# Kernel tuning notes

Measured on AMD Instinct MI355X. Metric: run time of the kernel, lower is better.

Reference implementation:

```python
import jax, jax.numpy as jnp
import numpy as np

B, C, Himg, Wimg = 4, 256, 64, 64
HID = 256
K = 8
EPS_NORM = 1e-12
BN_EPS = 1e-5


def setup_inputs() -> dict:
    key = jax.random.key(0)
    ks = jax.random.split(key, 14)
    s = lambda fan: 1.0 / np.sqrt(fan)
    inp = {
        "features": jax.random.normal(ks[0], (B, C, Himg, Wimg), dtype=jnp.float32),
        # HypergraphConv 0: theta (C->HID), phi (HID->HID). Weights stored [in,out].
        "theta0_w": jax.random.normal(ks[1], (C, HID), dtype=jnp.float32) * s(C),
        "theta0_b": jnp.zeros((HID,), jnp.float32),
        "phi0_w": jax.random.normal(ks[2], (HID, HID), dtype=jnp.float32) * s(HID),
        "phi0_b": jnp.zeros((HID,), jnp.float32),
        # HypergraphConv 1: theta (HID->HID), phi (HID->HID)
        "theta1_w": jax.random.normal(ks[3], (HID, HID), dtype=jnp.float32) * s(HID),
        "theta1_b": jnp.zeros((HID,), jnp.float32),
        "phi1_w": jax.random.normal(ks[4], (HID, HID), dtype=jnp.float32) * s(HID),
        "phi1_b": jnp.zeros((HID,), jnp.float32),
        # out_proj: 1x1 conv HID->C, stored as [HID, C]
        "proj_w": jax.random.normal(ks[5], (HID, C), dtype=jnp.float32) * s(HID),
        "proj_b": jnp.zeros((C,), jnp.float32),
        # BatchNorm2d affine params
        "bn_gamma": jnp.ones((C,), jnp.float32),
        "bn_beta": jnp.zeros((C,), jnp.float32),
    }
    return inp


def _build_hypergraph(features):
    # features: [B, C, H, W] -> nodes [B, N, C]; incidence from batch 0 only
    b, c, h, w = features.shape
    n = h * w
    feat_flat = features.reshape(b, c, n).transpose(0, 2, 1)  # [B, N, C]
    f0 = feat_flat[0]  # [N, C] (original computes full-batch similarity but uses [0])
    f0n = f0 / jnp.maximum(jnp.linalg.norm(f0, axis=-1, keepdims=True), EPS_NORM)
    sim = f0n @ f0n.T  # [N, N]
    _, idx = jax.lax.top_k(sim, K)  # [N, K]
    rows = idx.reshape(-1)
    cols = jnp.repeat(jnp.arange(n), K)
    Hm = jnp.zeros((n, n), jnp.float32).at[rows, cols].set(1.0)  # [N, E=N]
    # L1 column normalization (F.normalize p=1 dim=0)
    Hn = Hm / jnp.maximum(Hm.sum(axis=0, keepdims=True), EPS_NORM)
    return Hn, feat_flat


def _hconv(x, Hn, tw, tb, pw, pb):
    # x: [B, N, Cin]
    xt = x @ tw + tb  # [B, N, Cout]
    ef = jnp.einsum('ne,bnc->bec', Hn, xt)  # H^T @ x_theta -> edge feats
    xp = ef @ pw + pb  # [B, E, Cout]
    return jnp.einsum('ne,bec->bnc', Hn, xp)  # H @ x_phi


def reference(features, theta0_w, theta0_b, phi0_w, phi0_b,
              theta1_w, theta1_b, phi1_w, phi1_b,
              proj_w, proj_b, bn_gamma, bn_beta):
    b, c, h, w = features.shape
    Hn, x = _build_hypergraph(features)
    x = jax.nn.relu(_hconv(x, Hn, theta0_w, theta0_b, phi0_w, phi0_b))
    x = jax.nn.relu(_hconv(x, Hn, theta1_w, theta1_b, phi1_w, phi1_b)) + x
    # back to [B, HID, H, W] then 1x1 conv
    x = x.transpose(0, 2, 1).reshape(b, HID, h, w)
    x = jnp.einsum('bihw,io->bohw', x, proj_w) + proj_b[None, :, None, None]
    # BatchNorm2d (training mode: batch statistics, biased variance)
    mean = x.mean(axis=(0, 2, 3))
    var = x.var(axis=(0, 2, 3))
    xn = (x - mean[None, :, None, None]) * jax.lax.rsqrt(var + BN_EPS)[None, :, None, None]
    xn = xn * bn_gamma[None, :, None, None] + bn_beta[None, :, None, None]
    return features + xn
```

## Files before the change

### kernel.cpp

```cpp
#include <hip/hip_runtime.h>

namespace {

constexpr int NB = 4;
constexpr int NC = 256;
constexpr int NN = 4096;

typedef __attribute__((ext_vector_type(8))) short bf8;
typedef __attribute__((ext_vector_type(4))) float f4;
typedef unsigned short ushort_t;
typedef unsigned long long ull;

__device__ __forceinline__ float bf2f(unsigned short u) {
  return __uint_as_float(((unsigned)u) << 16);
}
__device__ __forceinline__ unsigned short f2bf(float f) {
  unsigned x = __float_as_uint(f);
  return (unsigned short)((x + 0x7FFFu + ((x >> 16) & 1u)) >> 16);
}

__device__ __forceinline__ unsigned enc_f(float f) {
  unsigned u = __float_as_uint(f);
  return (u & 0x80000000u) ? ~u : (u | 0x80000000u);
}

__device__ __forceinline__ void ins8(ull* b, ull k) {
  if (k <= b[7]) return;
  b[7] = k;
#pragma unroll
  for (int p = 7; p >= 1; --p) {
    if (b[p] > b[p-1]) { ull t = b[p]; b[p] = b[p-1]; b[p-1] = t; }
  }
}

__global__ __launch_bounds__(256) void norm_kernel(const float* __restrict__ feat,
                                                   float* __restrict__ inv,
                                                   int* __restrict__ counts,
                                                   float* __restrict__ bnsum) {
  int n = blockIdx.x * 256 + threadIdx.x;
  counts[n] = 0;
  if (n < 2 * NC) bnsum[n] = 0.f;
  float ss = 0.f;
  for (int c = 0; c < NC; ++c) { float v = feat[(size_t)c * NN + n]; ss = fmaf(v, v, ss); }
  inv[n] = 1.f / fmaxf(sqrtf(ss), 1e-12f);
}

__global__ __launch_bounds__(256) void xpose_split_kernel(const float* __restrict__ feat,
                                                          const float* __restrict__ inv,
                                                          unsigned short* __restrict__ Xhi,
                                                          unsigned short* __restrict__ Xlo) {
  __shared__ float tile[64][65];
  int n0 = blockIdx.x * 64, c0 = blockIdx.y * 64;
  int tid = threadIdx.x;
#pragma unroll
  for (int i = 0; i < 4; ++i) {
    int u = tid + i * 256; int cr = u >> 4, q = u & 15;
    float4 v = *(const float4*)&feat[(size_t)(c0 + cr) * NN + n0 + q * 4];
    tile[cr][q*4+0] = v.x; tile[cr][q*4+1] = v.y; tile[cr][q*4+2] = v.z; tile[cr][q*4+3] = v.w;
  }
  __syncthreads();
#pragma unroll
  for (int i = 0; i < 4; ++i) {
    int u = tid + i * 256; int nr = u >> 4, q = u & 15;
    float iv = inv[n0 + nr];
    ushort4 h, l;
    float x0 = tile[q*4+0][nr] * iv, x1 = tile[q*4+1][nr] * iv;
    float x2 = tile[q*4+2][nr] * iv, x3 = tile[q*4+3][nr] * iv;
    h.x = f2bf(x0); l.x = f2bf(x0 - bf2f(h.x));
    h.y = f2bf(x1); l.y = f2bf(x1 - bf2f(h.y));
    h.z = f2bf(x2); l.z = f2bf(x2 - bf2f(h.z));
    h.w = f2bf(x3); l.w = f2bf(x3 - bf2f(h.w));
    size_t o = (size_t)(n0 + nr) * NC + c0 + q * 4;
    *(ushort4*)&Xhi[o] = h;
    *(ushort4*)&Xlo[o] = l;
  }
}

__global__ __launch_bounds__(256) void wcvt_kernel(const float* __restrict__ w0,
                                                   const float* __restrict__ w1,
                                                   const float* __restrict__ w2,
                                                   const float* __restrict__ w3,
                                                   const float* __restrict__ w4,
                                                   unsigned short* __restrict__ Wt) {
  __shared__ float tile[64][65];
  int z = blockIdx.z;
  const float* W = (z == 0) ? w0 : (z == 1) ? w1 : (z == 2) ? w2 : (z == 3) ? w3 : w4;
  int k0 = blockIdx.x * 64, n0 = blockIdx.y * 64;
  int tid = threadIdx.x;
#pragma unroll
  for (int i = 0; i < 4; ++i) {
    int u = tid + i * 256; int kr = u >> 4, q = u & 15;
    float4 v = *(const float4*)&W[(size_t)(k0 + kr) * NC + n0 + q * 4];
    tile[kr][q*4+0] = v.x; tile[kr][q*4+1] = v.y; tile[kr][q*4+2] = v.z; tile[kr][q*4+3] = v.w;
  }
  __syncthreads();
#pragma unroll
  for (int i = 0; i < 4; ++i) {
    int u = tid + i * 256; int nr = u >> 4, q = u & 15;
    ushort4 o;
    o.x = f2bf(tile[q*4+0][nr]); o.y = f2bf(tile[q*4+1][nr]);
    o.z = f2bf(tile[q*4+2][nr]); o.w = f2bf(tile[q*4+3][nr]);
    *(ushort4*)&Wt[(size_t)z * 65536 + (size_t)(n0 + nr) * NC + k0 + q * 4] = o;
  }
}

__global__ __launch_bounds__(256) void feat2bf_kernel(const float* __restrict__ feat,
                                                      unsigned short* __restrict__ xin) {
  __shared__ float tile[64][65];
  int n0 = blockIdx.x * 64, c0 = blockIdx.y * 64, b = blockIdx.z;
  int tid = threadIdx.x;
#pragma unroll
  for (int i = 0; i < 4; ++i) {
    int u = tid + i * 256; int cr = u >> 4, q = u & 15;
    float4 v = *(const float4*)&feat[((size_t)b * NC + c0 + cr) * NN + n0 + q * 4];
    tile[cr][q*4+0] = v.x; tile[cr][q*4+1] = v.y; tile[cr][q*4+2] = v.z; tile[cr][q*4+3] = v.w;
  }
  __syncthreads();
#pragma unroll
  for (int i = 0; i < 4; ++i) {
    int u = tid + i * 256; int nr = u >> 4, q = u & 15;
    ushort4 o;
    o.x = f2bf(tile[q*4+0][nr]); o.y = f2bf(tile[q*4+1][nr]);
    o.z = f2bf(tile[q*4+2][nr]); o.w = f2bf(tile[q*4+3][nr]);
    *(ushort4*)&xin[((size_t)(b << 12) + n0 + nr) * NC + c0 + q * 4] = o;
  }
}

__global__ __launch_bounds__(256) void simtop_kernel(const unsigned short* __restrict__ Xhi,
                                                     const unsigned short* __restrict__ Xlo,
                                                     ull* __restrict__ cand) {
  __shared__ __align__(16) char lds[73728];
  ushort_t (*sAh)[72] = (ushort_t(*)[72])(lds);
  ushort_t (*sAl)[72] = (ushort_t(*)[72])(lds + 18432);
  ushort_t (*sBh)[72] = (ushort_t(*)[72])(lds + 36864);
  ushort_t (*sBl)[72] = (ushort_t(*)[72])(lds + 55296);
  float    (*simT)[132] = (float(*)[132])(lds);
  ull* scratch = (ull*)(lds);

  int tid = threadIdx.x, wave = tid >> 6, lane = tid & 63;
  int wm = wave >> 1, wn = wave & 1;
  int m0 = blockIdx.y * 128, n0 = blockIdx.x * 128;
  f4 acc[4][4];
#pragma unroll
  for (int i = 0; i < 4; ++i)
#pragma unroll
    for (int j = 0; j < 4; ++j) acc[i][j] = (f4){0.f, 0.f, 0.f, 0.f};

  for (int k0 = 0; k0 < NC; k0 += 64) {
#pragma unroll
    for (int i = 0; i < 4; ++i) {
      int u = tid + i * 256; int r = u >> 3, q = u & 7;
      size_t am = (size_t)(m0 + r) * NC + k0 + q * 8;
      size_t an = (size_t)(n0 + r) * NC + k0 + q * 8;
      *(uint4*)&sAh[r][q*8] = *(const uint4*)&Xhi[am];
      *(uint4*)&sAl[r][q*8] = *(const uint4*)&Xlo[am];
      *(uint4*)&sBh[r][q*8] = *(const uint4*)&Xhi[an];
      *(uint4*)&sBl[r][q*8] = *(const uint4*)&Xlo[an];
    }
    __syncthreads();
#pragma unroll
    for (int ks = 0; ks < 2; ++ks) {
      bf8 ah[4], al[4];
#pragma unroll
      for (int mf = 0; mf < 4; ++mf) {
        ah[mf] = *(const bf8*)&sAh[wm*64 + mf*16 + (lane & 15)][ks*32 + (lane >> 4)*8];
        al[mf] = *(const bf8*)&sAl[wm*64 + mf*16 + (lane & 15)][ks*32 + (lane >> 4)*8];
      }
#pragma unroll
      for (int nf = 0; nf < 4; ++nf) {
        bf8 bh = *(const bf8*)&sBh[wn*64 + nf*16 + (lane & 15)][ks*32 + (lane >> 4)*8];
        bf8 bl = *(const bf8*)&sBl[wn*64 + nf*16 + (lane & 15)][ks*32 + (lane >> 4)*8];
#pragma unroll
        for (int mf = 0; mf < 4; ++mf) {
          acc[mf][nf] = __builtin_amdgcn_mfma_f32_16x16x32_bf16(ah[mf], bh, acc[mf][nf], 0, 0, 0);
          acc[mf][nf] = __builtin_amdgcn_mfma_f32_16x16x32_bf16(ah[mf], bl, acc[mf][nf], 0, 0, 0);
          acc[mf][nf] = __builtin_amdgcn_mfma_f32_16x16x32_bf16(al[mf], bh, acc[mf][nf], 0, 0, 0);
        }
      }
    }
    __syncthreads();
  }

#pragma unroll
  for (int mf = 0; mf < 4; ++mf) {
#pragma unroll
    for (int nf = 0; nf < 4; ++nf) {
      int cl = wn*64 + nf*16 + (lane & 15);
#pragma unroll
      for (int r = 0; r < 4; ++r) {
        simT[wm*64 + mf*16 + (lane >> 4)*4 + r][cl] = acc[mf][nf][r];
      }
    }
  }
  __syncthreads();

  int r_loc = tid >> 1, h = tid & 1;
  const float* rowp = &simT[r_loc][h * 64];
  ull b8[8] = {0,0,0,0,0,0,0,0};
#pragma unroll
  for (int i = 0; i < 16; ++i) {
    float4 v = *(const float4*)(rowp + i * 4);
    int jb = n0 + h*64 + i*4;
    ins8(b8, ((ull)enc_f(v.x) << 32) | (ull)(0xFFFFFFFFu - (unsigned)(jb + 0)));
    ins8(b8, ((ull)enc_f(v.y) << 32) | (ull)(0xFFFFFFFFu - (unsigned)(jb + 1)));
    ins8(b8, ((ull)enc_f(v.z) << 32) | (ull)(0xFFFFFFFFu - (unsigned)(jb + 2)));
    ins8(b8, ((ull)enc_f(v.w) << 32) | (ull)(0xFFFFFFFFu - (unsigned)(jb + 3)));
  }
  __syncthreads();
  if (h) {
#pragma unroll
    for (int k = 0; k < 8; ++k) scratch[r_loc * 8 + k] = b8[k];
  }
  __syncthreads();
  if (!h) {
#pragma unroll
    for (int k = 0; k < 8; ++k) ins8(b8, scratch[r_loc * 8 + k]);
    ull* dst = cand + (size_t)(m0 + r_loc) * 256 + blockIdx.x * 8;
#pragma unroll
    for (int k = 0; k < 8; ++k) dst[k] = b8[k];
  }
}

__global__ __launch_bounds__(256) void merge_kernel(const ull* __restrict__ cand,
                                                    int* __restrict__ idx8,
                                                    int* __restrict__ counts) {
  int row = blockIdx.x * 256 + threadIdx.x;
  const ull* cp = cand + (size_t)row * 256;
  ull b8[8] = {0,0,0,0,0,0,0,0};
  for (int g = 0; g < 32; ++g) {
#pragma unroll 1
    for (int k = 0; k < 8; ++k) {
      ull key = cp[g * 8 + k];
      if (key <= b8[7]) break;
      ins8(b8, key);
    }
  }
#pragma unroll
  for (int k = 0; k < 8; ++k) {
    int j = (int)(0xFFFFFFFFu - (unsigned)(b8[k] & 0xFFFFFFFFull));
    idx8[row * 8 + k] = j;
    atomicAdd(&counts[j], 1);
  }
}

__global__ __launch_bounds__(256) void scan_kernel(const int* __restrict__ counts,
                                                   int* __restrict__ offsets,
                                                   int* __restrict__ cursor) {
  __shared__ int ssum[256];
  __shared__ int sbase[257];
  int t = threadIdx.x;
  int loc[16];
  int s = 0;
#pragma unroll
  for (int i = 0; i < 16; ++i) { loc[i] = s; s += counts[t*16 + i]; }
  ssum[t] = s;
  __syncthreads();
  if (t == 0) {
    int acc = 0;
    for (int i = 0; i < 256; ++i) { sbase[i] = acc; acc += ssum[i]; }
    sbase[256] = acc;
  }
  __syncthreads();
  int b0 = sbase[t];
#pragma unroll
  for (int i = 0; i < 16; ++i) {
    int off = b0 + loc[i];
    offsets[t*16 + i] = off;
    cursor [t*16 + i] = off;
  }
  if (t == 0) offsets[NN] = sbase[256];
}

__global__ __launch_bounds__(256) void fill_kernel(const int* __restrict__ idx8,
                                                   int* __restrict__ cursor,
                                                   int* __restrict__ edgelist) {
  int t = blockIdx.x * 256 + threadIdx.x;
  int n = idx8[t];
  int pos = atomicAdd(&cursor[n], 1);
  edgelist[pos] = t >> 3;
}

template<int OUTF32, int BNS>
__global__ __launch_bounds__(512) void gemm_bf16_kernel(const unsigned short* __restrict__ A,
                                                        const unsigned short* __restrict__ Wt,
                                                        const float* __restrict__ bias,
                                                        void* __restrict__ outp,
                                                        float* __restrict__ bnsum) {
  __shared__ ushort_t sA[128][72];
  __shared__ ushort_t sB[128][72];
  int tid = threadIdx.x, wave = tid >> 6, lane = tid & 63;
  int wm = wave >> 2, wn = wave & 3;
  int n0 = blockIdx.x * 128, m0 = blockIdx.y * 128;
  f4 acc[4][2];
#pragma unroll
  for (int i = 0; i < 4; ++i)
#pragma unroll
    for (int j = 0; j < 2; ++j) acc[i][j] = (f4){0.f, 0.f, 0.f, 0.f};

  for (int k0 = 0; k0 < NC; k0 += 64) {
#pragma unroll
    for (int i = 0; i < 2; ++i) {
      int u = tid + i * 512; int r = u >> 3, q = u & 7;
      *(uint4*)&sA[r][q*8] = *(const uint4*)&A [(size_t)(m0 + r) * NC + k0 + q * 8];
      *(uint4*)&sB[r][q*8] = *(const uint4*)&Wt[(size_t)(n0 + r) * NC + k0 + q * 8];
    }
    __syncthreads();
#pragma unroll
    for (int ks = 0; ks < 2; ++ks) {
      bf8 a[4], b[2];
#pragma unroll
      for (int mf = 0; mf < 4; ++mf)
        a[mf] = *(const bf8*)&sA[wm*64 + mf*16 + (lane & 15)][ks*32 + (lane >> 4)*8];
#pragma unroll
      for (int nf = 0; nf < 2; ++nf)
        b[nf] = *(const bf8*)&sB[wn*32 + nf*16 + (lane & 15)][ks*32 + (lane >> 4)*8];
#pragma unroll
      for (int nf = 0; nf < 2; ++nf)
#pragma unroll
        for (int mf = 0; mf < 4; ++mf)
          acc[mf][nf] = __builtin_amdgcn_mfma_f32_16x16x32_bf16(a[mf], b[nf], acc[mf][nf], 0, 0, 0);
    }
    __syncthreads();
  }
#pragma unroll
  for (int nf = 0; nf < 2; ++nf) {
    int n = n0 + wn*32 + nf*16 + (lane & 15);
    float bi = bias[n];
    float s1 = 0.f, s2 = 0.f;
#pragma unroll
    for (int mf = 0; mf < 4; ++mf) {
#pragma unroll
      for (int r = 0; r < 4; ++r) {
        int m = m0 + wm*64 + mf*16 + (lane >> 4)*4 + r;
        float v = acc[mf][nf][r] + bi;
        if (OUTF32) ((float*)outp)[(size_t)m * NC + n] = v;
        else ((unsigned short*)outp)[(size_t)m * NC + n] = f2bf(v);
        if (BNS) { s1 += v; s2 = fmaf(v, v, s2); }
      }
    }
    if (BNS) {
      s1 += __shfl_xor(s1, 16); s1 += __shfl_xor(s1, 32);
      s2 += __shfl_xor(s2, 16); s2 += __shfl_xor(s2, 32);
      if (lane < 16) {
        atomicAdd(&bnsum[n], s1);
        atomicAdd(&bnsum[NC + n], s2);
      }
    }
  }
}

__global__ __launch_bounds__(256) void gather_kernel(const unsigned short* __restrict__ xt,
                                                     const int* __restrict__ idx8,
                                                     unsigned short* __restrict__ ef) {
  int b = blockIdx.y;
  int e = blockIdx.x * 4 + (threadIdx.x >> 6);
  int lane = threadIdx.x & 63;
  float s0 = 0, s1 = 0, s2 = 0, s3 = 0;
  const int* ip = &idx8[e * 8];
#pragma unroll
  for (int k = 0; k < 8; ++k) {
    int n = ip[k];
    uint2 v = *(const uint2*)&xt[((size_t)((b << 12) + n)) * NC + lane * 4];
    s0 += bf2f((unsigned short)(v.x & 0xFFFF)); s1 += bf2f((unsigned short)(v.x >> 16));
    s2 += bf2f((unsigned short)(v.y & 0xFFFF)); s3 += bf2f((unsigned short)(v.y >> 16));
  }
  uint2 o;
  o.x = (unsigned)f2bf(s0 * 0.125f) | ((unsigned)f2bf(s1 * 0.125f) << 16);
  o.y = (unsigned)f2bf(s2 * 0.125f) | ((unsigned)f2bf(s3 * 0.125f) << 16);
  *(uint2*)&ef[((size_t)((b << 12) + e)) * NC + lane * 4] = o;
}

template<int MODE>
__global__ __launch_bounds__(256) void scatter_kernel(const unsigned short* __restrict__ xp,
                                                      const int* __restrict__ offsets,
                                                      const int* __restrict__ edgelist,
                                                      const unsigned short* __restrict__ res,
                                                      unsigned short* __restrict__ outb) {
  int b = blockIdx.y;
  int n = blockIdx.x * 4 + (threadIdx.x >> 6);
  int lane = threadIdx.x & 63;
  int s0i = offsets[n], s1i = offsets[n + 1];
  float s0 = 0, s1 = 0, s2 = 0, s3 = 0;
  for (int j = s0i; j < s1i; ++j) {
    int e = edgelist[j];
    uint2 v = *(const uint2*)&xp[((size_t)((b << 12) + e)) * NC + lane * 4];
    s0 += bf2f((unsigned short)(v.x & 0xFFFF)); s1 += bf2f((unsigned short)(v.x >> 16));
    s2 += bf2f((unsigned short)(v.y & 0xFFFF)); s3 += bf2f((unsigned short)(v.y >> 16));
  }
  s0 = fmaxf(s0 * 0.125f, 0.f); s1 = fmaxf(s1 * 0.125f, 0.f);
  s2 = fmaxf(s2 * 0.125f, 0.f); s3 = fmaxf(s3 * 0.125f, 0.f);
  size_t o = ((size_t)((b << 12) + n)) * NC + lane * 4;
  if (MODE == 1) {
    uint2 v = *(const uint2*)&res[o];
    s0 += bf2f((unsigned short)(v.x & 0xFFFF)); s1 += bf2f((unsigned short)(v.x >> 16));
    s2 += bf2f((unsigned short)(v.y & 0xFFFF)); s3 += bf2f((unsigned short)(v.y >> 16));
  }
  uint2 ov;
  ov.x = (unsigned)f2bf(s0) | ((unsigned)f2bf(s1) << 16);
  ov.y = (unsigned)f2bf(s2) | ((unsigned)f2bf(s3) << 16);
  *(uint2*)&outb[o] = ov;
}

__global__ __launch_bounds__(256) void final_kernel(const float* __restrict__ y,
                                                    const float* __restrict__ feat,
                                                    const float* __restrict__ bnsum,
                                                    const float* __restrict__ gam,
                                                    const float* __restrict__ bet,
                                                    float* __restrict__ out) {
  __shared__ float tile[64][65];
  __shared__ float sa_[64], sb_[64];
  int n0 = blockIdx.x * 64;
  int c0 = blockIdx.y * 64;
  int b  = blockIdx.z;
  int tid = threadIdx.x;
  if (tid < 64) {
    const float invn = 1.f / (float)(NB * NN);
    int c = c0 + tid;
    float mean = bnsum[c] * invn;
    float var  = bnsum[NC + c] * invn - mean * mean;
    float a = gam[c] * rsqrtf(var + 1e-5f);
    sa_[tid] = a;
    sb_[tid] = bet[c] - mean * a;
  }
  int n_l = tid >> 2;
  int q   = tid & 3;
  const float4* y4 = (const float4*)y;
#pragma unroll
  for (int i = 0; i < 4; ++i) {
    int cl = q * 16 + i * 4;
    float4 v = y4[(size_t)(b * NN + n0 + n_l) * 64 + ((c0 + cl) >> 2)];
    tile[n_l][cl+0] = v.x; tile[n_l][cl+1] = v.y; tile[n_l][cl+2] = v.z; tile[n_l][cl+3] = v.w;
  }
  __syncthreads();
  int cl2 = tid >> 6;
  int nl2 = tid & 63;
#pragma unroll
  for (int p = 0; p < 16; ++p) {
    int ci = p * 4 + cl2;
    float a = sa_[ci], bb = sb_[ci];
    size_t o = (size_t)b * (NC * NN) + (size_t)(c0 + ci) * NN + n0 + nl2;
    out[o] = feat[o] + fmaf(a, tile[nl2][ci], bb);
  }
}

}

extern "C" void kernel_launch(void* const* d_in, const int* in_sizes, int n_in,
                              void* d_out, int out_size, void* d_ws, size_t ws_size,
                              hipStream_t stream) {
  (void)in_sizes; (void)n_in; (void)out_size; (void)ws_size;
  const float* feat = (const float*)d_in[0];
  const float* t0w  = (const float*)d_in[1];
  const float* t0b  = (const float*)d_in[2];
  const float* p0w  = (const float*)d_in[3];
  const float* p0b  = (const float*)d_in[4];
  const float* t1w  = (const float*)d_in[5];
  const float* t1b  = (const float*)d_in[6];
  const float* p1w  = (const float*)d_in[7];
  const float* p1b  = (const float*)d_in[8];
  const float* pw   = (const float*)d_in[9];
  const float* pb   = (const float*)d_in[10];
  const float* gam  = (const float*)d_in[11];
  const float* bet  = (const float*)d_in[12];
  float* out = (float*)d_out;

  char* ws = (char*)d_ws;
  float*          y   = (float*)ws;
  unsigned short* xin = (unsigned short*)(ws + (16u << 20));
  unsigned short* xt  = (unsigned short*)(ws + (24u << 20));
  unsigned short* ef  = (unsigned short*)(ws + (32u << 20));
  unsigned short* xp  = (unsigned short*)(ws + (40u << 20));
  unsigned short* x1  = (unsigned short*)(ws + (48u << 20));
  unsigned short* x2  = (unsigned short*)(ws + (56u << 20));
  unsigned short* Xhi = (unsigned short*)(ws + (64u << 20));
  unsigned short* Xlo = (unsigned short*)(ws + (66u << 20));
  ull*            cand = (ull*)(ws + (68u << 20));
  char* sm = ws + (76u << 20);
  unsigned short* Wt  = (unsigned short*)sm;
  int*   idx8     = (int*)(sm + 655360);
  int*   counts   = (int*)(sm + 786432);
  int*   offsets  = (int*)(sm + 802816);
  int*   cursor   = (int*)(sm + 819456);
  int*   edgelist = (int*)(sm + 835840);
  float* inv      = (float*)(sm + 966912);
  float* bnsum    = (float*)(sm + 983296);

  norm_kernel<<<NN / 256, 256, 0, stream>>>(feat, inv, counts, bnsum);
  xpose_split_kernel<<<dim3(64, 4), 256, 0, stream>>>(feat, inv, Xhi, Xlo);
  wcvt_kernel<<<dim3(4, 4, 5), 256, 0, stream>>>(t0w, p0w, t1w, p1w, pw, Wt);
  feat2bf_kernel<<<dim3(64, 4, 4), 256, 0, stream>>>(feat, xin);

  simtop_kernel<<<dim3(32, 32), 256, 0, stream>>>(Xhi, Xlo, cand);
  merge_kernel<<<16, 256, 0, stream>>>(cand, idx8, counts);
  scan_kernel<<<1, 256, 0, stream>>>(counts, offsets, cursor);
  fill_kernel<<<128, 256, 0, stream>>>(idx8, cursor, edgelist);

  gemm_bf16_kernel<0,0><<<dim3(2, 128), 512, 0, stream>>>(xin, Wt + 0*65536, t0b, xt, nullptr);
  gather_kernel<<<dim3(1024, 4), 256, 0, stream>>>(xt, idx8, ef);
  gemm_bf16_kernel<0,0><<<dim3(2, 128), 512, 0, stream>>>(ef, Wt + 1*65536, p0b, xp, nullptr);
  scatter_kernel<0><<<dim3(1024, 4), 256, 0, stream>>>(xp, offsets, edgelist, nullptr, x1);
  gemm_bf16_kernel<0,0><<<dim3(2, 128), 512, 0, stream>>>(x1, Wt + 2*65536, t1b, xt, nullptr);
  gather_kernel<<<dim3(1024, 4), 256, 0, stream>>>(xt, idx8, ef);
  gemm_bf16_kernel<0,0><<<dim3(2, 128), 512, 0, stream>>>(ef, Wt + 3*65536, p1b, xp, nullptr);
  scatter_kernel<1><<<dim3(1024, 4), 256, 0, stream>>>(xp, offsets, edgelist, x1, x2);
  gemm_bf16_kernel<1,1><<<dim3(2, 128), 512, 0, stream>>>(x2, Wt + 4*65536, pb, y, bnsum);

  final_kernel<<<dim3(64, 4, 4), 256, 0, stream>>>(y, feat, bnsum, gam, bet, out);
}
```

Before: 369.5 us.

## Exploit similarity symmetry, fuse gather into GEMM, swizzle LDS, parallelize top-k merge

The similarity/top-k kernel now computes only the upper-triangular tiles and uses each tile twice, once for row candidates and once for column candidates via a transposed scan, which halves the split-bf16 MFMA work. It moves to 512-thread blocks with XOR-swizzled LDS and a shuffle-based 4-way top-8 merge. The merge kernel splits each row across 8 lanes and combines them with shuffles. The edge-feature gather is fused into the A-tile load of the phi GEMM, which removes two kernels and the ef round trip. Risks include extra per-block gather latency inside the GEMM, because each tile is re-gathered for every N block, and serial column scans on LDS.

```diff
diff --git a/kernel.cpp b/kernel.cpp
--- a/kernel.cpp
+++ b/kernel.cpp
@@ -18,7 +18,6 @@
   unsigned x = __float_as_uint(f);
   return (unsigned short)((x + 0x7FFFu + ((x >> 16) & 1u)) >> 16);
 }
-
 __device__ __forceinline__ unsigned enc_f(float f) {
   unsigned u = __float_as_uint(f);
   return (u & 0x80000000u) ? ~u : (u | 0x80000000u);
@@ -30,6 +29,25 @@
 #pragma unroll
   for (int p = 7; p >= 1; --p) {
     if (b[p] > b[p-1]) { ull t = b[p]; b[p] = b[p-1]; b[p-1] = t; }
+  }
+}
+
+__device__ __forceinline__ ull shfl_xor_ull(ull v, int mask) {
+  unsigned lo = (unsigned)(v & 0xFFFFFFFFull), hi = (unsigned)(v >> 32);
+  lo = (unsigned)__shfl_xor((int)lo, mask);
+  hi = (unsigned)__shfl_xor((int)hi, mask);
+  return ((ull)hi << 32) | (ull)lo;
+}
+
+template<int MAXS>
+__device__ __forceinline__ void shfl_merge8(ull* b) {
+#pragma unroll
+  for (int s = 1; s <= MAXS; s <<= 1) {
+    ull tmp[8];
+#pragma unroll
+    for (int k = 0; k < 8; ++k) tmp[k] = shfl_xor_ull(b[k], s);
+#pragma unroll
+    for (int k = 0; k < 8; ++k) ins8(b, tmp[k]);
   }
 }
 
@@ -126,7 +144,7 @@
   }
 }
 
-__global__ __launch_bounds__(256) void simtop_kernel(const unsigned short* __restrict__ Xhi,
+__global__ __launch_bounds__(512) void simtop_kernel(const unsigned short* __restrict__ Xhi,
                                                      const unsigned short* __restrict__ Xlo,
                                                      ull* __restrict__ cand) {
   __shared__ __align__(16) char lds[73728];
@@ -135,99 +153,123 @@
   ushort_t (*sBh)[72] = (ushort_t(*)[72])(lds + 36864);
   ushort_t (*sBl)[72] = (ushort_t(*)[72])(lds + 55296);
   float    (*simT)[132] = (float(*)[132])(lds);
-  ull* scratch = (ull*)(lds);
 
   int tid = threadIdx.x, wave = tid >> 6, lane = tid & 63;
-  int wm = wave >> 1, wn = wave & 1;
-  int m0 = blockIdx.y * 128, n0 = blockIdx.x * 128;
-  f4 acc[4][4];
+  int wm = wave >> 2, wn = wave & 3;
+  int bid = blockIdx.x;
+  int pi = (int)((sqrtf(8.f * (float)bid + 1.f) - 1.f) * 0.5f);
+  while ((pi + 1) * (pi + 2) / 2 <= bid) ++pi;
+  while (pi * (pi + 1) / 2 > bid) --pi;
+  int pj = bid - pi * (pi + 1) / 2;
+  int m0 = pj * 128, n0 = pi * 128;
+
+  f4 acc[4][2];
 #pragma unroll
   for (int i = 0; i < 4; ++i)
 #pragma unroll
-    for (int j = 0; j < 4; ++j) acc[i][j] = (f4){0.f, 0.f, 0.f, 0.f};
+    for (int j = 0; j < 2; ++j) acc[i][j] = (f4){0.f, 0.f, 0.f, 0.f};
 
   for (int k0 = 0; k0 < NC; k0 += 64) {
 #pragma unroll
-    for (int i = 0; i < 4; ++i) {
-      int u = tid + i * 256; int r = u >> 3, q = u & 7;
+    for (int i = 0; i < 2; ++i) {
+      int u = tid + i * 512; int r = u >> 3, q = u & 7;
+      int qp = (q ^ ((r >> 1) & 7)) * 8;
       size_t am = (size_t)(m0 + r) * NC + k0 + q * 8;
       size_t an = (size_t)(n0 + r) * NC + k0 + q * 8;
-      *(uint4*)&sAh[r][q*8] = *(const uint4*)&Xhi[am];
-      *(uint4*)&sAl[r][q*8] = *(const uint4*)&Xlo[am];
-      *(uint4*)&sBh[r][q*8] = *(const uint4*)&Xhi[an];
-      *(uint4*)&sBl[r][q*8] = *(const uint4*)&Xlo[an];
+      *(uint4*)&sAh[r][qp] = *(const uint4*)&Xhi[am];
+      *(uint4*)&sAl[r][qp] = *(const uint4*)&Xlo[am];
+      *(uint4*)&sBh[r][qp] = *(const uint4*)&Xhi[an];
+      *(uint4*)&sBl[r][qp] = *(const uint4*)&Xlo[an];
     }
     __syncthreads();
 #pragma unroll
     for (int ks = 0; ks < 2; ++ks) {
-      bf8 ah[4], al[4];
+      int qr = ks * 4 + (lane >> 4);
+      bf8 ah[4], al[4], bh[2], bl[2];
 #pragma unroll
       for (int mf = 0; mf < 4; ++mf) {
-        ah[mf] = *(const bf8*)&sAh[wm*64 + mf*16 + (lane & 15)][ks*32 + (lane >> 4)*8];
-        al[mf] = *(const bf8*)&sAl[wm*64 + mf*16 + (lane & 15)][ks*32 + (lane >> 4)*8];
-      }
-#pragma unroll
-      for (int nf = 0; nf < 4; ++nf) {
-        bf8 bh = *(const bf8*)&sBh[wn*64 + nf*16 + (lane & 15)][ks*32 + (lane >> 4)*8];
-        bf8 bl = *(const bf8*)&sBl[wn*64 + nf*16 + (lane & 15)][ks*32 + (lane >> 4)*8];
+        int rr = wm*64 + mf*16 + (lane & 15);
+        int qp = (qr ^ ((rr >> 1) & 7)) * 8;
+        ah[mf] = *(const bf8*)&sAh[rr][qp];
+        al[mf] = *(const bf8*)&sAl[rr][qp];
+      }
+#pragma unroll
+      for (int nf = 0; nf < 2; ++nf) {
+        int rr = wn*32 + nf*16 + (lane & 15);
+        int qp = (qr ^ ((rr >> 1) & 7)) * 8;
+        bh[nf] = *(const bf8*)&sBh[rr][qp];
+        bl[nf] = *(const bf8*)&sBl[rr][qp];
+      }
+#pragma unroll
+      for (int nf = 0; nf < 2; ++nf)
 #pragma unroll
         for (int mf = 0; mf < 4; ++mf) {
-          acc[mf][nf] = __builtin_amdgcn_mfma_f32_16x16x32_bf16(ah[mf], bh, acc[mf][nf], 0, 0, 0);
-          acc[mf][nf] = __builtin_amdgcn_mfma_f32_16x16x32_bf16(ah[mf], bl, acc[mf][nf], 0, 0, 0);
-          acc[mf][nf] = __builtin_amdgcn_mfma_f32_16x16x32_bf16(al[mf], bh, acc[mf][nf], 0, 0, 0);
+          acc[mf][nf] = __builtin_amdgcn_mfma_f32_16x16x32_bf16(ah[mf], bh[nf], acc[mf][nf], 0, 0, 0);
+          acc[mf][nf] = __builtin_amdgcn_mfma_f32_16x16x32_bf16(ah[mf], bl[nf], acc[mf][nf], 0, 0, 0);
+          acc[mf][nf] = __builtin_amdgcn_mfma_f32_16x16x32_bf16(al[mf], bh[nf], acc[mf][nf], 0, 0, 0);
         }
-      }
     }
     __syncthreads();
   }
 
 #pragma unroll
-  for (int mf = 0; mf < 4; ++mf) {
-#pragma unroll
-    for (int nf = 0; nf < 4; ++nf) {
-      int cl = wn*64 + nf*16 + (lane & 15);
-#pragma unroll
-      for (int r = 0; r < 4; ++r) {
+  for (int mf = 0; mf < 4; ++mf)
+#pragma unroll
+    for (int nf = 0; nf < 2; ++nf) {
+      int cl = wn*32 + nf*16 + (lane & 15);
+#pragma unroll
+      for (int r = 0; r < 4; ++r)
         simT[wm*64 + mf*16 + (lane >> 4)*4 + r][cl] = acc[mf][nf][r];
-      }
-    }
-  }
-  __syncthreads();
-
-  int r_loc = tid >> 1, h = tid & 1;
-  const float* rowp = &simT[r_loc][h * 64];
-  ull b8[8] = {0,0,0,0,0,0,0,0};
-#pragma unroll
-  for (int i = 0; i < 16; ++i) {
-    float4 v = *(const float4*)(rowp + i * 4);
-    int jb = n0 + h*64 + i*4;
-    ins8(b8, ((ull)enc_f(v.x) << 32) | (ull)(0xFFFFFFFFu - (unsigned)(jb + 0)));
-    ins8(b8, ((ull)enc_f(v.y) << 32) | (ull)(0xFFFFFFFFu - (unsigned)(jb + 1)));
-    ins8(b8, ((ull)enc_f(v.z) << 32) | (ull)(0xFFFFFFFFu - (unsigned)(jb + 2)));
-    ins8(b8, ((ull)enc_f(v.w) << 32) | (ull)(0xFFFFFFFFu - (unsigned)(jb + 3)));
-  }
-  __syncthreads();
-  if (h) {
-#pragma unroll
-    for (int k = 0; k < 8; ++k) scratch[r_loc * 8 + k] = b8[k];
-  }
-  __syncthreads();
-  if (!h) {
-#pragma unroll
-    for (int k = 0; k < 8; ++k) ins8(b8, scratch[r_loc * 8 + k]);
-    ull* dst = cand + (size_t)(m0 + r_loc) * 256 + blockIdx.x * 8;
-#pragma unroll
-    for (int k = 0; k < 8; ++k) dst[k] = b8[k];
+    }
+  __syncthreads();
+
+  {
+    int rrow = tid >> 2, q4 = tid & 3;
+    ull b8[8] = {0,0,0,0,0,0,0,0};
+#pragma unroll
+    for (int i = 0; i < 8; ++i) {
+      int cofs = q4 * 32 + (((i + q4 * 2) & 7)) * 4;
+      float4 v = *(const float4*)&simT[rrow][cofs];
+      int jb = n0 + cofs;
+      ins8(b8, ((ull)enc_f(v.x) << 32) | (ull)(0xFFFFFFFFu - (unsigned)(jb + 0)));
+      ins8(b8, ((ull)enc_f(v.y) << 32) | (ull)(0xFFFFFFFFu - (unsigned)(jb + 1)));
+      ins8(b8, ((ull)enc_f(v.z) << 32) | (ull)(0xFFFFFFFFu - (unsigned)(jb + 2)));
+      ins8(b8, ((ull)enc_f(v.w) << 32) | (ull)(0xFFFFFFFFu - (unsigned)(jb + 3)));
+    }
+    shfl_merge8<2>(b8);
+    if (q4 == 0) {
+      ull* dst = cand + (size_t)(m0 + rrow) * 256 + pi * 8;
+#pragma unroll
+      for (int k = 0; k < 8; ++k) dst[k] = b8[k];
+    }
+  }
+
+  if (pi != pj) {
+    int ccol = tid >> 2, seg = tid & 3;
+    ull c8[8] = {0,0,0,0,0,0,0,0};
+    for (int i = 0; i < 32; ++i) {
+      int rr = seg * 32 + ((i + seg) & 31);
+      float v = simT[rr][ccol];
+      int jb = m0 + rr;
+      ins8(c8, ((ull)enc_f(v) << 32) | (ull)(0xFFFFFFFFu - (unsigned)jb));
+    }
+    shfl_merge8<2>(c8);
+    if (seg == 0) {
+      ull* dst = cand + (size_t)(n0 + ccol) * 256 + pj * 8;
+#pragma unroll
+      for (int k = 0; k < 8; ++k) dst[k] = c8[k];
+    }
   }
 }
 
 __global__ __launch_bounds__(256) void merge_kernel(const ull* __restrict__ cand,
                                                     int* __restrict__ idx8,
                                                     int* __restrict__ counts) {
-  int row = blockIdx.x * 256 + threadIdx.x;
-  const ull* cp = cand + (size_t)row * 256;
+  int t = blockIdx.x * 256 + threadIdx.x;
+  int row = t >> 3, part = t & 7;
+  const ull* cp = cand + (size_t)row * 256 + part * 32;
   ull b8[8] = {0,0,0,0,0,0,0,0};
-  for (int g = 0; g < 32; ++g) {
+  for (int g = 0; g < 4; ++g) {
 #pragma unroll 1
     for (int k = 0; k < 8; ++k) {
       ull key = cp[g * 8 + k];
@@ -235,11 +277,14 @@
       ins8(b8, key);
     }
   }
-#pragma unroll
-  for (int k = 0; k < 8; ++k) {
-    int j = (int)(0xFFFFFFFFu - (unsigned)(b8[k] & 0xFFFFFFFFull));
-    idx8[row * 8 + k] = j;
-    atomicAdd(&counts[j], 1);
+  shfl_merge8<4>(b8);
+  if (part == 0) {
+#pragma unroll
+    for (int k = 0; k < 8; ++k) {
+      int j = (int)(0xFFFFFFFFu - (unsigned)(b8[k] & 0xFFFFFFFFull));
+      idx8[row * 8 + k] = j;
+      atomicAdd(&counts[j], 1);
+    }
   }
 }
 
@@ -280,17 +325,27 @@
   edgelist[pos] = t >> 3;
 }
 
-template<int OUTF32, int BNS>
+template<int OUTF32, int BNS, int GATHER>
 __global__ __launch_bounds__(512) void gemm_bf16_kernel(const unsigned short* __restrict__ A,
                                                         const unsigned short* __restrict__ Wt,
                                                         const float* __restrict__ bias,
                                                         void* __restrict__ outp,
-                                                        float* __restrict__ bnsum) {
+                                                        float* __restrict__ bnsum,
+                                                        const int* __restrict__ idx8) {
   __shared__ ushort_t sA[128][72];
   __shared__ ushort_t sB[128][72];
+  __shared__ int sIdx[128][8];
   int tid = threadIdx.x, wave = tid >> 6, lane = tid & 63;
   int wm = wave >> 2, wn = wave & 3;
   int n0 = blockIdx.x * 128, m0 = blockIdx.y * 128;
+  size_t bbase = 0;
+  if constexpr (GATHER) {
+    int e0 = m0 & 4095;
+    bbase = ((size_t)(m0 >> 12) << 12) * NC;
+#pragma unroll
+    for (int u = tid; u < 1024; u += 512) ((int*)sIdx)[u] = idx8[e0 * 8 + u];
+    __syncthreads();
+  }
   f4 acc[4][2];
 #pragma unroll
   for (int i = 0; i < 4; ++i)
@@ -301,19 +356,44 @@
 #pragma unroll
     for (int i = 0; i < 2; ++i) {
       int u = tid + i * 512; int r = u >> 3, q = u & 7;
-      *(uint4*)&sA[r][q*8] = *(const uint4*)&A [(size_t)(m0 + r) * NC + k0 + q * 8];
-      *(uint4*)&sB[r][q*8] = *(const uint4*)&Wt[(size_t)(n0 + r) * NC + k0 + q * 8];
+      int qp = (q ^ ((r >> 1) & 7)) * 8;
+      if constexpr (GATHER) {
+        float s[8] = {0.f,0.f,0.f,0.f,0.f,0.f,0.f,0.f};
+#pragma unroll
+        for (int k = 0; k < 8; ++k) {
+          int nn = sIdx[r][k];
+          uint4 v = *(const uint4*)&A[bbase + (size_t)nn * NC + k0 + q * 8];
+          s[0] += bf2f((unsigned short)(v.x & 0xFFFF)); s[1] += bf2f((unsigned short)(v.x >> 16));
+          s[2] += bf2f((unsigned short)(v.y & 0xFFFF)); s[3] += bf2f((unsigned short)(v.y >> 16));
+          s[4] += bf2f((unsigned short)(v.z & 0xFFFF)); s[5] += bf2f((unsigned short)(v.z >> 16));
+          s[6] += bf2f((unsigned short)(v.w & 0xFFFF)); s[7] += bf2f((unsigned short)(v.w >> 16));
+        }
+        uint4 o;
+        o.x = (unsigned)f2bf(s[0]*0.125f) | ((unsigned)f2bf(s[1]*0.125f) << 16);
+        o.y = (unsigned)f2bf(s[2]*0.125f) | ((unsigned)f2bf(s[3]*0.125f) << 16);
+        o.z = (unsigned)f2bf(s[4]*0.125f) | ((unsigned)f2bf(s[5]*0.125f) << 16);
+        o.w = (unsigned)f2bf(s[6]*0.125f) | ((unsigned)f2bf(s[7]*0.125f) << 16);
+        *(uint4*)&sA[r][qp] = o;
+      } else {
+        *(uint4*)&sA[r][qp] = *(const uint4*)&A[(size_t)(m0 + r) * NC + k0 + q * 8];
+      }
+      *(uint4*)&sB[r][qp] = *(const uint4*)&Wt[(size_t)(n0 + r) * NC + k0 + q * 8];
     }
     __syncthreads();
 #pragma unroll
     for (int ks = 0; ks < 2; ++ks) {
+      int qr = ks * 4 + (lane >> 4);
       bf8 a[4], b[2];
 #pragma unroll
-      for (int mf = 0; mf < 4; ++mf)
-        a[mf] = *(const bf8*)&sA[wm*64 + mf*16 + (lane & 15)][ks*32 + (lane >> 4)*8];
-#pragma unroll
-      for (int nf = 0; nf < 2; ++nf)
-        b[nf] = *(const bf8*)&sB[wn*32 + nf*16 + (lane & 15)][ks*32 + (lane >> 4)*8];
+      for (int mf = 0; mf < 4; ++mf) {
+        int rr = wm*64 + mf*16 + (lane & 15);
+        a[mf] = *(const bf8*)&sA[rr][(qr ^ ((rr >> 1) & 7)) * 8];
+      }
+#pragma unroll
+      for (int nf = 0; nf < 2; ++nf) {
+        int rr = wn*32 + nf*16 + (lane & 15);
+        b[nf] = *(const bf8*)&sB[rr][(qr ^ ((rr >> 1) & 7)) * 8];
+      }
 #pragma unroll
       for (int nf = 0; nf < 2; ++nf)
 #pragma unroll
@@ -347,27 +427,6 @@
       }
     }
   }
-}
-
-__global__ __launch_bounds__(256) void gather_kernel(const unsigned short* __restrict__ xt,
-                                                     const int* __restrict__ idx8,
-                                                     unsigned short* __restrict__ ef) {
-  int b = blockIdx.y;
-  int e = blockIdx.x * 4 + (threadIdx.x >> 6);
-  int lane = threadIdx.x & 63;
-  float s0 = 0, s1 = 0, s2 = 0, s3 = 0;
-  const int* ip = &idx8[e * 8];
-#pragma unroll
-  for (int k = 0; k < 8; ++k) {
-    int n = ip[k];
-    uint2 v = *(const uint2*)&xt[((size_t)((b << 12) + n)) * NC + lane * 4];
-    s0 += bf2f((unsigned short)(v.x & 0xFFFF)); s1 += bf2f((unsigned short)(v.x >> 16));
-    s2 += bf2f((unsigned short)(v.y & 0xFFFF)); s3 += bf2f((unsigned short)(v.y >> 16));
-  }
-  uint2 o;
-  o.x = (unsigned)f2bf(s0 * 0.125f) | ((unsigned)f2bf(s1 * 0.125f) << 16);
-  o.y = (unsigned)f2bf(s2 * 0.125f) | ((unsigned)f2bf(s3 * 0.125f) << 16);
-  *(uint2*)&ef[((size_t)((b << 12) + e)) * NC + lane * 4] = o;
 }
 
 template<int MODE>
@@ -468,7 +527,6 @@
   float*          y   = (float*)ws;
   unsigned short* xin = (unsigned short*)(ws + (16u << 20));
   unsigned short* xt  = (unsigned short*)(ws + (24u << 20));
-  unsigned short* ef  = (unsigned short*)(ws + (32u << 20));
   unsigned short* xp  = (unsigned short*)(ws + (40u << 20));
   unsigned short* x1  = (unsigned short*)(ws + (48u << 20));
   unsigned short* x2  = (unsigned short*)(ws + (56u << 20));
@@ -490,20 +548,18 @@
   wcvt_kernel<<<dim3(4, 4, 5), 256, 0, stream>>>(t0w, p0w, t1w, p1w, pw, Wt);
   feat2bf_kernel<<<dim3(64, 4, 4), 256, 0, stream>>>(feat, xin);
 
-  simtop_kernel<<<dim3(32, 32), 256, 0, stream>>>(Xhi, Xlo, cand);
-  merge_kernel<<<16, 256, 0, stream>>>(cand, idx8, counts);
+  simtop_kernel<<<528, 512, 0, stream>>>(Xhi, Xlo, cand);
+  merge_kernel<<<128, 256, 0, stream>>>(cand, idx8, counts);
   scan_kernel<<<1, 256, 0, stream>>>(counts, offsets, cursor);
   fill_kernel<<<128, 256, 0, stream>>>(idx8, cursor, edgelist);
 
-  gemm_bf16_kernel<0,0><<<dim3(2, 128), 512, 0, stream>>>(xin, Wt + 0*65536, t0b, xt, nullptr);
-  gather_kernel<<<dim3(1024, 4), 256, 0, stream>>>(xt, idx8, ef);
-  gemm_bf16_kernel<0,0><<<dim3(2, 128), 512, 0, stream>>>(ef, Wt + 1*65536, p0b, xp, nullptr);
+  gemm_bf16_kernel<0,0,0><<<dim3(2, 128), 512, 0, stream>>>(xin, Wt + 0*65536, t0b, xt, nullptr, nullptr);
+  gemm_bf16_kernel<0,0,1><<<dim3(2, 128), 512, 0, stream>>>(xt,  Wt + 1*65536, p0b, xp, nullptr, idx8);
   scatter_kernel<0><<<dim3(1024, 4), 256, 0, stream>>>(xp, offsets, edgelist, nullptr, x1);
-  gemm_bf16_kernel<0,0><<<dim3(2, 128), 512, 0, stream>>>(x1, Wt + 2*65536, t1b, xt, nullptr);
-  gather_kernel<<<dim3(1024, 4), 256, 0, stream>>>(xt, idx8, ef);
-  gemm_bf16_kernel<0,0><<<dim3(2, 128), 512, 0, stream>>>(ef, Wt + 3*65536, p1b, xp, nullptr);
+  gemm_bf16_kernel<0,0,0><<<dim3(2, 128), 512, 0, stream>>>(x1, Wt + 2*65536, t1b, xt, nullptr, nullptr);
+  gemm_bf16_kernel<0,0,1><<<dim3(2, 128), 512, 0, stream>>>(xt, Wt + 3*65536, p1b, xp, nullptr, idx8);
   scatter_kernel<1><<<dim3(1024, 4), 256, 0, stream>>>(xp, offsets, edgelist, x1, x2);
-  gemm_bf16_kernel<1,1><<<dim3(2, 128), 512, 0, stream>>>(x2, Wt + 4*65536, pb, y, bnsum);
+  gemm_bf16_kernel<1,1,0><<<dim3(2, 128), 512, 0, stream>>>(x2, Wt + 4*65536, pb, y, bnsum, nullptr);
 
   final_kernel<<<dim3(64, 4, 4), 256, 0, stream>>>(y, feat, bnsum, gam, bet, out);
 }
```

Result: faster. 334.1 us (-9.6%).
